# Kernel tuning notes

Hardware: AMD Instinct MI355X
Metric: run time of the kernel (lower is better)

Reference implementation:

```python
import jax, jax.numpy as jnp
import numpy as np

E = 1024   # emb_dim
H = 1024   # hidden_size
L = 2      # num_layers
V = 50257  # vocab_size
S = 2048   # encoder input length
T = 2048   # decoder target length


def setup_inputs() -> dict:
    key = jax.random.key(0)
    ks = jax.random.split(key, 16)
    s = 0.02  # init scale
    f32 = jnp.float32
    return {
        "inputs": jax.random.randint(ks[0], (1, S), 0, V),
        "outputs": jax.random.randint(ks[1], (1, T), 0, V),
        "sos": 1,
        "enc_emb": jax.random.normal(ks[2], (V, E), f32) * s,
        "dec_emb": jax.random.normal(ks[3], (V, E), f32) * s,
        # Stacked LSTM weights; layer-0 input dim == E == H so layers stack.
        "enc_Wih": jax.random.normal(ks[4], (L, 4 * H, H), f32) * s,
        "enc_Whh": jax.random.normal(ks[5], (L, 4 * H, H), f32) * s,
        "enc_bih": jax.random.normal(ks[6], (L, 4 * H), f32) * s,
        "enc_bhh": jax.random.normal(ks[7], (L, 4 * H), f32) * s,
        "dec_Wih": jax.random.normal(ks[8], (L, 4 * H, H), f32) * s,
        "dec_Whh": jax.random.normal(ks[9], (L, 4 * H, H), f32) * s,
        "dec_bih": jax.random.normal(ks[10], (L, 4 * H), f32) * s,
        "dec_bhh": jax.random.normal(ks[11], (L, 4 * H), f32) * s,
        "lin_W": jax.random.normal(ks[12], (V, H), f32) * s,
        "lin_b": jax.random.normal(ks[13], (V,), f32) * s,
    }


def _run_stack(xs, Wih, Whh, bih, bhh, h0, c0):
    # xs: [S, E]; Wih/Whh: [L, 4H, H]; h0/c0: [L, H]
    # PyTorch LSTM gate order: i, f, g, o.
    h_fin, c_fin = [], []
    for l in range(Wih.shape[0]):
        Wi, Wh, bi, bh = Wih[l], Whh[l], bih[l], bhh[l]

        def step(carry, x, Wi=Wi, Wh=Wh, bi=bi, bh=bh):
            h, c = carry
            g = Wi @ x + bi + Wh @ h + bh           # [4H]
            i, f, gg, o = jnp.split(g, 4)
            c = jax.nn.sigmoid(f) * c + jax.nn.sigmoid(i) * jnp.tanh(gg)
            h = jax.nn.sigmoid(o) * jnp.tanh(c)
            return (h, c), h

        (h, c), xs = jax.lax.scan(step, (h0[l], c0[l]), xs)
        h_fin.append(h)
        c_fin.append(c)
    return xs, jnp.stack(h_fin), jnp.stack(c_fin)


def reference(inputs, outputs, sos, enc_emb, dec_emb,
              enc_Wih, enc_Whh, enc_bih, enc_bhh,
              dec_Wih, dec_Whh, dec_bih, dec_bhh,
              lin_W, lin_b):
    # Encoder over the source sequence (batch == 1, squeezed away).
    x = enc_emb[inputs[0]]                       # [S, E]
    z = jnp.zeros((L, H), dtype=x.dtype)
    _, hN, cN = _run_stack(x, enc_Wih, enc_Whh, enc_bih, enc_bhh, z, z)
    # Full teacher forcing: decoder inputs are [sos, outputs[:, :-1]].
    dec_tokens = jnp.concatenate(
        [jnp.array([sos], dtype=outputs.dtype), outputs[0, :-1]])
    y = dec_emb[dec_tokens]                      # [T, E]
    dec_out, _, _ = _run_stack(y, dec_Wih, dec_Whh, dec_bih, dec_bhh, hN, cN)
    logits = dec_out @ lin_W.T + lin_b           # [T, V]
    return logits
```

## Files before the change

### kernel.cpp

```cpp
#include <hip/hip_runtime.h>
#include <hip/hip_bf16.h>
#include <math.h>

#define S_LEN 2048
#define T_LEN 2048
#define HID   1024
#define GATES 4096
#define VOCAB 50257
#define NWG2  192
#define RECT  512

typedef unsigned long long ull;

__device__ __forceinline__ float sigmoidf_(float x) { return 1.0f / (1.0f + expf(-x)); }

__global__ void zero_f32(float* __restrict__ p, int n) {
  int i = blockIdx.x * blockDim.x + threadIdx.x;
  if (i < n) p[i] = 0.0f;
}

__global__ void zero_f4(float4* __restrict__ p, size_t n4) {
  size_t i = (size_t)blockIdx.x * blockDim.x + threadIdx.x;
  size_t stride = (size_t)gridDim.x * blockDim.x;
  for (; i < n4; i += stride) p[i] = make_float4(0.f, 0.f, 0.f, 0.f);
}

__global__ void build_dec_tokens(const int* __restrict__ outputs, const int* __restrict__ sos,
                                 int* __restrict__ toks, int T) {
  int t = blockIdx.x * blockDim.x + threadIdx.x;
  if (t < T) toks[t] = (t == 0) ? sos[0] : outputs[t - 1];
}

__global__ void gather_rows(const float* __restrict__ emb, const int* __restrict__ toks,
                            float* __restrict__ out) {
  int row = blockIdx.x;
  int tok = toks[row];
  const float4* src = (const float4*)(emb + (size_t)tok * HID);
  float4* dst = (float4*)(out + (size_t)row * HID);
  dst[threadIdx.x] = src[threadIdx.x];
}

__global__ __launch_bounds__(256) void gemm_xwt(
    const float* __restrict__ X, const float* __restrict__ W,
    const float* __restrict__ b1, const float* __restrict__ b2,
    float* __restrict__ C, int M, int N, int K)
{
  __shared__ float Xs[16][68];
  __shared__ float Ws[16][68];
  const int tid = threadIdx.x;
  const int tx = tid & 15;
  const int ty = tid >> 4;
  const int m0 = blockIdx.y * 64;
  const int n0 = blockIdx.x * 64;
  const int lr = tid >> 2;
  const int lc = (tid & 3) * 4;
  float acc[4][4] = {{0.f}};

  for (int k0 = 0; k0 < K; k0 += 16) {
    float4 xv = *(const float4*)(X + (size_t)(m0 + lr) * K + k0 + lc);
    float4 wv = make_float4(0.f, 0.f, 0.f, 0.f);
    int wr = n0 + lr;
    if (wr < N) wv = *(const float4*)(W + (size_t)wr * K + k0 + lc);
    __syncthreads();
    Xs[lc + 0][lr] = xv.x; Xs[lc + 1][lr] = xv.y; Xs[lc + 2][lr] = xv.z; Xs[lc + 3][lr] = xv.w;
    Ws[lc + 0][lr] = wv.x; Ws[lc + 1][lr] = wv.y; Ws[lc + 2][lr] = wv.z; Ws[lc + 3][lr] = wv.w;
    __syncthreads();
#pragma unroll
    for (int kk = 0; kk < 16; ++kk) {
      float4 a = *(const float4*)&Xs[kk][ty * 4];
      float4 b = *(const float4*)&Ws[kk][tx * 4];
      float av[4] = {a.x, a.y, a.z, a.w};
      float bv[4] = {b.x, b.y, b.z, b.w};
#pragma unroll
      for (int i = 0; i < 4; ++i)
#pragma unroll
        for (int j = 0; j < 4; ++j)
          acc[i][j] = fmaf(av[i], bv[j], acc[i][j]);
    }
  }
#pragma unroll
  for (int i = 0; i < 4; ++i) {
    int m = m0 + ty * 4 + i;
#pragma unroll
    for (int j = 0; j < 4; ++j) {
      int n = n0 + tx * 4 + j;
      if (n < N) {
        float bias = 0.f;
        if (b1) bias += b1[n];
        if (b2) bias += b2[n];
        C[(size_t)m * N + n] = acc[i][j] + bias;
      }
    }
  }
}

__global__ __launch_bounds__(RECT, 2) void lstm2(
    const float* __restrict__ A,   const float* __restrict__ Wh0,
    const float* __restrict__ Wi1, const float* __restrict__ Wh1,
    const float* __restrict__ bi1, const float* __restrict__ bh1,
    const float* __restrict__ h00, const float* __restrict__ c00,
    const float* __restrict__ h01, const float* __restrict__ c01,
    ull* __restrict__ s0, ull* __restrict__ s1,
    float* __restrict__ hf0, float* __restrict__ cf0,
    float* __restrict__ hf1, float* __restrict__ cf1,
    float* __restrict__ dec_out, int T)
{
  const int tid = threadIdx.x;
  const int wg = blockIdx.x;

  __shared__ float lds_x[HID];
  __shared__ float lds_h[HID];
  __shared__ float lds_g[64];
  __shared__ float lds_c[16];

  if (wg < 64) {
    const int lane8 = tid & 7;
    const int rloc = tid >> 3;
    const int jloc = rloc & 15;
    const int gate = rloc >> 4;
    const int grow = gate * HID + wg * 16 + jloc;

    float4 Wr[32];
    {
      const float4* wrow = (const float4*)(Wh0 + (size_t)grow * HID);
#pragma unroll
      for (int i = 0; i < 32; ++i) Wr[i] = wrow[lane8 + i * 8];
    }

    if (tid < 16) lds_c[tid] = c00[wg * 16 + tid];
    if (tid < 256) ((float4*)lds_h)[tid] = ((const float4*)h00)[tid];
    __syncthreads();

    float areg = (lane8 == 0) ? A[grow] : 0.f;

    for (int t = 0; t < T; ++t) {
      if (t > 0) {
        const ull* hb = s0 + (size_t)(t - 1) * HID;
        ull v0 = __hip_atomic_load(&hb[2 * tid],     __ATOMIC_RELAXED, __HIP_MEMORY_SCOPE_AGENT);
        ull v1 = __hip_atomic_load(&hb[2 * tid + 1], __ATOMIC_RELAXED, __HIP_MEMORY_SCOPE_AGENT);
        while ((unsigned)(v0 >> 32) < (unsigned)t)
          v0 = __hip_atomic_load(&hb[2 * tid],     __ATOMIC_RELAXED, __HIP_MEMORY_SCOPE_AGENT);
        while ((unsigned)(v1 >> 32) < (unsigned)t)
          v1 = __hip_atomic_load(&hb[2 * tid + 1], __ATOMIC_RELAXED, __HIP_MEMORY_SCOPE_AGENT);
        lds_h[2 * tid]     = __uint_as_float((unsigned)v0);
        lds_h[2 * tid + 1] = __uint_as_float((unsigned)v1);
        __syncthreads();
      }

      const float aval = areg;
      if (lane8 == 0 && t + 1 < T) areg = A[(size_t)(t + 1) * GATES + grow];

      float p0 = 0.f, p1 = 0.f, p2 = 0.f, p3 = 0.f;
#pragma unroll
      for (int i = 0; i < 32; ++i) {
        const float4 hv = *(const float4*)&lds_h[(lane8 << 2) + (i << 5)];
        p0 = fmaf(Wr[i].x, hv.x, p0);
        p1 = fmaf(Wr[i].y, hv.y, p1);
        p2 = fmaf(Wr[i].z, hv.z, p2);
        p3 = fmaf(Wr[i].w, hv.w, p3);
      }
      float sum = (p0 + p1) + (p2 + p3);
      sum += __shfl_xor(sum, 1);
      sum += __shfl_xor(sum, 2);
      sum += __shfl_xor(sum, 4);
      if (lane8 == 0) lds_g[rloc] = sum + aval;
      __syncthreads();

      if (tid < 16) {
        const float gi = lds_g[tid];
        const float gf = lds_g[16 + tid];
        const float gg = lds_g[32 + tid];
        const float go = lds_g[48 + tid];
        const float c = sigmoidf_(gf) * lds_c[tid] + sigmoidf_(gi) * tanhf(gg);
        const float h = sigmoidf_(go) * tanhf(c);
        lds_c[tid] = c;
        const int col = wg * 16 + tid;
        const ull pk = ((ull)(unsigned)(t + 1) << 32) | (ull)__float_as_uint(h);
        __hip_atomic_store(&s0[(size_t)t * HID + col], pk,
                           __ATOMIC_RELAXED, __HIP_MEMORY_SCOPE_AGENT);
        if (t == T - 1) {
          if (hf0) hf0[col] = h;
          if (cf0) cf0[col] = c;
        }
      }
    }
  } else {
    const int wg1 = wg - 64;
    const int lane16 = tid & 15;
    const int rloc = tid >> 4;
    const int jloc = rloc & 7;
    const int gate = rloc >> 3;
    const int grow = gate * HID + wg1 * 8 + jloc;

    float4 Wir[16], Whr[16];
    {
      const float4* wi = (const float4*)(Wi1 + (size_t)grow * HID);
      const float4* wh = (const float4*)(Wh1 + (size_t)grow * HID);
#pragma unroll
      for (int i = 0; i < 16; ++i) {
        Wir[i] = wi[lane16 + i * 16];
        Whr[i] = wh[lane16 + i * 16];
      }
    }
    const float breg = bi1[grow] + bh1[grow];

    if (tid < 8) lds_c[tid] = c01[wg1 * 8 + tid];
    if (tid < 256) ((float4*)lds_h)[tid] = ((const float4*)h01)[tid];
    __syncthreads();

    for (int t = 0; t < T; ++t) {
      if (t > 0) {
        const ull* hb = s1 + (size_t)(t - 1) * HID;
        ull v0 = __hip_atomic_load(&hb[2 * tid],     __ATOMIC_RELAXED, __HIP_MEMORY_SCOPE_AGENT);
        ull v1 = __hip_atomic_load(&hb[2 * tid + 1], __ATOMIC_RELAXED, __HIP_MEMORY_SCOPE_AGENT);
        while ((unsigned)(v0 >> 32) < (unsigned)t)
          v0 = __hip_atomic_load(&hb[2 * tid],     __ATOMIC_RELAXED, __HIP_MEMORY_SCOPE_AGENT);
        while ((unsigned)(v1 >> 32) < (unsigned)t)
          v1 = __hip_atomic_load(&hb[2 * tid + 1], __ATOMIC_RELAXED, __HIP_MEMORY_SCOPE_AGENT);
        lds_h[2 * tid]     = __uint_as_float((unsigned)v0);
        lds_h[2 * tid + 1] = __uint_as_float((unsigned)v1);
      }
      {
        const ull* xb = s0 + (size_t)t * HID;
        ull v0 = __hip_atomic_load(&xb[2 * tid],     __ATOMIC_RELAXED, __HIP_MEMORY_SCOPE_AGENT);
        ull v1 = __hip_atomic_load(&xb[2 * tid + 1], __ATOMIC_RELAXED, __HIP_MEMORY_SCOPE_AGENT);
        while ((unsigned)(v0 >> 32) < (unsigned)(t + 1))
          v0 = __hip_atomic_load(&xb[2 * tid],     __ATOMIC_RELAXED, __HIP_MEMORY_SCOPE_AGENT);
        while ((unsigned)(v1 >> 32) < (unsigned)(t + 1))
          v1 = __hip_atomic_load(&xb[2 * tid + 1], __ATOMIC_RELAXED, __HIP_MEMORY_SCOPE_AGENT);
        lds_x[2 * tid]     = __uint_as_float((unsigned)v0);
        lds_x[2 * tid + 1] = __uint_as_float((unsigned)v1);
      }
      __syncthreads();

      float p0 = 0.f, p1 = 0.f, p2 = 0.f, p3 = 0.f;
#pragma unroll
      for (int i = 0; i < 16; ++i) {
        const float4 hv = *(const float4*)&lds_h[(lane16 << 2) + (i << 6)];
        p0 = fmaf(Whr[i].x, hv.x, p0);
        p1 = fmaf(Whr[i].y, hv.y, p1);
        p2 = fmaf(Whr[i].z, hv.z, p2);
        p3 = fmaf(Whr[i].w, hv.w, p3);
      }
#pragma unroll
      for (int i = 0; i < 16; ++i) {
        const float4 xv = *(const float4*)&lds_x[(lane16 << 2) + (i << 6)];
        p0 = fmaf(Wir[i].x, xv.x, p0);
        p1 = fmaf(Wir[i].y, xv.y, p1);
        p2 = fmaf(Wir[i].z, xv.z, p2);
        p3 = fmaf(Wir[i].w, xv.w, p3);
      }
      float sum = (p0 + p1) + (p2 + p3);
      sum += __shfl_xor(sum, 1);
      sum += __shfl_xor(sum, 2);
      sum += __shfl_xor(sum, 4);
      sum += __shfl_xor(sum, 8);
      if (lane16 == 0) lds_g[rloc] = sum + breg;
      __syncthreads();

      if (tid < 8) {
        const float gi = lds_g[tid];
        const float gf = lds_g[8 + tid];
        const float gg = lds_g[16 + tid];
        const float go = lds_g[24 + tid];
        const float c = sigmoidf_(gf) * lds_c[tid] + sigmoidf_(gi) * tanhf(gg);
        const float h = sigmoidf_(go) * tanhf(c);
        lds_c[tid] = c;
        const int col = wg1 * 8 + tid;
        const ull pk = ((ull)(unsigned)(t + 1) << 32) | (ull)__float_as_uint(h);
        __hip_atomic_store(&s1[(size_t)t * HID + col], pk,
                           __ATOMIC_RELAXED, __HIP_MEMORY_SCOPE_AGENT);
        if (dec_out) dec_out[(size_t)t * HID + col] = h;
        if (t == T - 1) {
          if (hf1) hf1[col] = h;
          if (cf1) cf1[col] = c;
        }
      }
    }
  }
}

extern "C" void kernel_launch(void* const* d_in, const int* in_sizes, int n_in,
                              void* d_out, int out_size, void* d_ws, size_t ws_size,
                              hipStream_t stream) {
  const int*   inputs  = (const int*)d_in[0];
  const int*   outputs = (const int*)d_in[1];
  const int*   sos     = (const int*)d_in[2];
  const float* enc_emb = (const float*)d_in[3];
  const float* dec_emb = (const float*)d_in[4];
  const float* enc_Wih = (const float*)d_in[5];
  const float* enc_Whh = (const float*)d_in[6];
  const float* enc_bih = (const float*)d_in[7];
  const float* enc_bhh = (const float*)d_in[8];
  const float* dec_Wih = (const float*)d_in[9];
  const float* dec_Whh = (const float*)d_in[10];
  const float* dec_bih = (const float*)d_in[11];
  const float* dec_bhh = (const float*)d_in[12];
  const float* lin_W   = (const float*)d_in[13];
  const float* lin_b   = (const float*)d_in[14];

  float* out = (float*)d_out;
  float* A_enc = out;
  float* A_dec = out + 8388608;
  ull*   s0e   = (ull*)(out + 16777216);
  ull*   s1e   = s0e + 2097152;
  ull*   s0d   = s1e + 2097152;
  ull*   s1d   = s0d + 2097152;

  char* ws = (char*)d_ws;
  float* zerosv = (float*)(ws + 0);
  float* hf0    = (float*)(ws + 4096);
  float* cf0    = (float*)(ws + 8192);
  float* hf1    = (float*)(ws + 12288);
  float* cf1    = (float*)(ws + 16384);
  int*   dtoks  = (int*)(ws + 20480);
  float* B1 = (float*)(ws + ((size_t)1  << 20));
  float* B3 = (float*)(ws + ((size_t)10 << 20));
  float* B2 = (float*)(ws + ((size_t)19 << 20));

  const size_t WOFF = (size_t)GATES * HID;
  const dim3 gemm_blk(256);
  const dim3 gemmA_grid(GATES / 64, S_LEN / 64);
  const dim3 gemmV_grid((VOCAB + 63) / 64, T_LEN / 64);

  zero_f4<<<2048, 256, 0, stream>>>((float4*)(out + 16777216), 4194304);
  zero_f32<<<4, 256, 0, stream>>>(zerosv, 1024);
  build_dec_tokens<<<8, 256, 0, stream>>>(outputs, sos, dtoks, T_LEN);

  gather_rows<<<S_LEN, 256, 0, stream>>>(enc_emb, inputs, B1);
  gemm_xwt<<<gemmA_grid, gemm_blk, 0, stream>>>(B1, enc_Wih, enc_bih, enc_bhh, A_enc, S_LEN, GATES, HID);
  gather_rows<<<T_LEN, 256, 0, stream>>>(dec_emb, dtoks, B3);
  gemm_xwt<<<gemmA_grid, gemm_blk, 0, stream>>>(B3, dec_Wih, dec_bih, dec_bhh, A_dec, T_LEN, GATES, HID);

  lstm2<<<NWG2, RECT, 0, stream>>>(
      A_enc, enc_Whh, enc_Wih + WOFF, enc_Whh + WOFF, enc_bih + GATES, enc_bhh + GATES,
      zerosv, zerosv, zerosv, zerosv, s0e, s1e, hf0, cf0, hf1, cf1, nullptr, S_LEN);

  lstm2<<<NWG2, RECT, 0, stream>>>(
      A_dec, dec_Whh, dec_Wih + WOFF, dec_Whh + WOFF, dec_bih + GATES, dec_bhh + GATES,
      hf0, cf0, hf1, cf1, s0d, s1d, nullptr, nullptr, nullptr, nullptr, B2, T_LEN);

  gemm_xwt<<<gemmV_grid, gemm_blk, 0, stream>>>(B2, lin_W, lin_b, nullptr, out, T_LEN, VOCAB, HID);
}
```

Before: 13.97 ms.

## Replace per-element tagged h exchange with per-workgroup flags and vector loads

The cross-workgroup handoff of hidden states changes from 64-bit value+step words, each polled by a spin loop, to plain float arrays plus one ready flag per workgroup per step. Consumers spin on a single flag and then fetch four floats with one cache-bypassing dwordx4 load, so each step moves less data and issues fewer atomic polls. Producers wait for their stores to complete before raising the flag, which adds ordering cost on the store side. Gate activations also switch to fast __expf-based sigmoid and tanh, which can lose some accuracy.

```diff
diff --git a/kernel.cpp b/kernel.cpp
--- a/kernel.cpp
+++ b/kernel.cpp
@@ -10,19 +10,21 @@
 #define NWG2  192
 #define RECT  512
 
-typedef unsigned long long ull;
-
-__device__ __forceinline__ float sigmoidf_(float x) { return 1.0f / (1.0f + expf(-x)); }
-
-__global__ void zero_f32(float* __restrict__ p, int n) {
+typedef unsigned int u32;
+
+__device__ __forceinline__ float fsig_(float x)  { return 1.0f / (1.0f + __expf(-x)); }
+__device__ __forceinline__ float ftanh_(float x) { float e = __expf(2.0f * x); return 1.0f - 2.0f / (e + 1.0f); }
+
+__device__ __forceinline__ float4 load_coherent4(const float* p) {
+  float4 v;
+  asm volatile("global_load_dwordx4 %0, %1, off sc0 sc1\n\ts_waitcnt vmcnt(0)"
+               : "=v"(v) : "v"(p) : "memory");
+  return v;
+}
+
+__global__ void zero_u32(u32* __restrict__ p, int n) {
   int i = blockIdx.x * blockDim.x + threadIdx.x;
-  if (i < n) p[i] = 0.0f;
-}
-
-__global__ void zero_f4(float4* __restrict__ p, size_t n4) {
-  size_t i = (size_t)blockIdx.x * blockDim.x + threadIdx.x;
-  size_t stride = (size_t)gridDim.x * blockDim.x;
-  for (; i < n4; i += stride) p[i] = make_float4(0.f, 0.f, 0.f, 0.f);
+  if (i < n) p[i] = 0u;
 }
 
 __global__ void build_dec_tokens(const int* __restrict__ outputs, const int* __restrict__ sos,
@@ -100,7 +102,8 @@
     const float* __restrict__ bi1, const float* __restrict__ bh1,
     const float* __restrict__ h00, const float* __restrict__ c00,
     const float* __restrict__ h01, const float* __restrict__ c01,
-    ull* __restrict__ s0, ull* __restrict__ s1,
+    float* __restrict__ s0, float* __restrict__ s1,
+    u32* __restrict__ t0, u32* __restrict__ t1,
     float* __restrict__ hf0, float* __restrict__ cf0,
     float* __restrict__ hf1, float* __restrict__ cf1,
     float* __restrict__ dec_out, int T)
@@ -135,15 +138,13 @@
 
     for (int t = 0; t < T; ++t) {
       if (t > 0) {
-        const ull* hb = s0 + (size_t)(t - 1) * HID;
-        ull v0 = __hip_atomic_load(&hb[2 * tid],     __ATOMIC_RELAXED, __HIP_MEMORY_SCOPE_AGENT);
-        ull v1 = __hip_atomic_load(&hb[2 * tid + 1], __ATOMIC_RELAXED, __HIP_MEMORY_SCOPE_AGENT);
-        while ((unsigned)(v0 >> 32) < (unsigned)t)
-          v0 = __hip_atomic_load(&hb[2 * tid],     __ATOMIC_RELAXED, __HIP_MEMORY_SCOPE_AGENT);
-        while ((unsigned)(v1 >> 32) < (unsigned)t)
-          v1 = __hip_atomic_load(&hb[2 * tid + 1], __ATOMIC_RELAXED, __HIP_MEMORY_SCOPE_AGENT);
-        lds_h[2 * tid]     = __uint_as_float((unsigned)v0);
-        lds_h[2 * tid + 1] = __uint_as_float((unsigned)v1);
+        if (tid < 256) {
+          const int c4 = tid << 2;
+          const u32* tg = t0 + (size_t)(t - 1) * 64 + (c4 >> 4);
+          while (__hip_atomic_load(tg, __ATOMIC_RELAXED, __HIP_MEMORY_SCOPE_AGENT) < (u32)t) {}
+          const float4 v = load_coherent4(s0 + (size_t)(t - 1) * HID + c4);
+          *(float4*)&lds_h[c4] = v;
+        }
         __syncthreads();
       }
 
@@ -171,17 +172,20 @@
         const float gf = lds_g[16 + tid];
         const float gg = lds_g[32 + tid];
         const float go = lds_g[48 + tid];
-        const float c = sigmoidf_(gf) * lds_c[tid] + sigmoidf_(gi) * tanhf(gg);
-        const float h = sigmoidf_(go) * tanhf(c);
+        const float c = fsig_(gf) * lds_c[tid] + fsig_(gi) * ftanh_(gg);
+        const float h = fsig_(go) * ftanh_(c);
         lds_c[tid] = c;
         const int col = wg * 16 + tid;
-        const ull pk = ((ull)(unsigned)(t + 1) << 32) | (ull)__float_as_uint(h);
-        __hip_atomic_store(&s0[(size_t)t * HID + col], pk,
+        __hip_atomic_store((u32*)&s0[(size_t)t * HID + col], __float_as_uint(h),
                            __ATOMIC_RELAXED, __HIP_MEMORY_SCOPE_AGENT);
         if (t == T - 1) {
           if (hf0) hf0[col] = h;
           if (cf0) cf0[col] = c;
         }
+        asm volatile("s_waitcnt vmcnt(0)" ::: "memory");
+        if (tid == 0)
+          __hip_atomic_store(&t0[(size_t)t * 64 + wg], (u32)(t + 1),
+                             __ATOMIC_RELAXED, __HIP_MEMORY_SCOPE_AGENT);
       }
     }
   } else {
@@ -209,27 +213,19 @@
     __syncthreads();
 
     for (int t = 0; t < T; ++t) {
-      if (t > 0) {
-        const ull* hb = s1 + (size_t)(t - 1) * HID;
-        ull v0 = __hip_atomic_load(&hb[2 * tid],     __ATOMIC_RELAXED, __HIP_MEMORY_SCOPE_AGENT);
-        ull v1 = __hip_atomic_load(&hb[2 * tid + 1], __ATOMIC_RELAXED, __HIP_MEMORY_SCOPE_AGENT);
-        while ((unsigned)(v0 >> 32) < (unsigned)t)
-          v0 = __hip_atomic_load(&hb[2 * tid],     __ATOMIC_RELAXED, __HIP_MEMORY_SCOPE_AGENT);
-        while ((unsigned)(v1 >> 32) < (unsigned)t)
-          v1 = __hip_atomic_load(&hb[2 * tid + 1], __ATOMIC_RELAXED, __HIP_MEMORY_SCOPE_AGENT);
-        lds_h[2 * tid]     = __uint_as_float((unsigned)v0);
-        lds_h[2 * tid + 1] = __uint_as_float((unsigned)v1);
-      }
-      {
-        const ull* xb = s0 + (size_t)t * HID;
-        ull v0 = __hip_atomic_load(&xb[2 * tid],     __ATOMIC_RELAXED, __HIP_MEMORY_SCOPE_AGENT);
-        ull v1 = __hip_atomic_load(&xb[2 * tid + 1], __ATOMIC_RELAXED, __HIP_MEMORY_SCOPE_AGENT);
-        while ((unsigned)(v0 >> 32) < (unsigned)(t + 1))
-          v0 = __hip_atomic_load(&xb[2 * tid],     __ATOMIC_RELAXED, __HIP_MEMORY_SCOPE_AGENT);
-        while ((unsigned)(v1 >> 32) < (unsigned)(t + 1))
-          v1 = __hip_atomic_load(&xb[2 * tid + 1], __ATOMIC_RELAXED, __HIP_MEMORY_SCOPE_AGENT);
-        lds_x[2 * tid]     = __uint_as_float((unsigned)v0);
-        lds_x[2 * tid + 1] = __uint_as_float((unsigned)v1);
+      if (tid < 256) {
+        const int c4 = tid << 2;
+        const u32* tg = t0 + (size_t)t * 64 + (c4 >> 4);
+        while (__hip_atomic_load(tg, __ATOMIC_RELAXED, __HIP_MEMORY_SCOPE_AGENT) < (u32)(t + 1)) {}
+        const float4 v = load_coherent4(s0 + (size_t)t * HID + c4);
+        *(float4*)&lds_x[c4] = v;
+      } else if (t > 0) {
+        const int u = tid - 256;
+        const int c4 = u << 2;
+        const u32* tg = t1 + (size_t)(t - 1) * 128 + (u >> 1);
+        while (__hip_atomic_load(tg, __ATOMIC_RELAXED, __HIP_MEMORY_SCOPE_AGENT) < (u32)t) {}
+        const float4 v = load_coherent4(s1 + (size_t)(t - 1) * HID + c4);
+        *(float4*)&lds_h[c4] = v;
       }
       __syncthreads();
 
@@ -263,18 +259,21 @@
         const float gf = lds_g[8 + tid];
         const float gg = lds_g[16 + tid];
         const float go = lds_g[24 + tid];
-        const float c = sigmoidf_(gf) * lds_c[tid] + sigmoidf_(gi) * tanhf(gg);
-        const float h = sigmoidf_(go) * tanhf(c);
+        const float c = fsig_(gf) * lds_c[tid] + fsig_(gi) * ftanh_(gg);
+        const float h = fsig_(go) * ftanh_(c);
         lds_c[tid] = c;
         const int col = wg1 * 8 + tid;
-        const ull pk = ((ull)(unsigned)(t + 1) << 32) | (ull)__float_as_uint(h);
-        __hip_atomic_store(&s1[(size_t)t * HID + col], pk,
+        __hip_atomic_store((u32*)&s1[(size_t)t * HID + col], __float_as_uint(h),
                            __ATOMIC_RELAXED, __HIP_MEMORY_SCOPE_AGENT);
         if (dec_out) dec_out[(size_t)t * HID + col] = h;
         if (t == T - 1) {
           if (hf1) hf1[col] = h;
           if (cf1) cf1[col] = c;
         }
+        asm volatile("s_waitcnt vmcnt(0)" ::: "memory");
+        if (tid == 0)
+          __hip_atomic_store(&t1[(size_t)t * 128 + wg1], (u32)(t + 1),
+                             __ATOMIC_RELAXED, __HIP_MEMORY_SCOPE_AGENT);
       }
     }
   }
@@ -302,10 +301,16 @@
   float* out = (float*)d_out;
   float* A_enc = out;
   float* A_dec = out + 8388608;
-  ull*   s0e   = (ull*)(out + 16777216);
-  ull*   s1e   = s0e + 2097152;
-  ull*   s0d   = s1e + 2097152;
-  ull*   s1d   = s0d + 2097152;
+  float* s0e   = out + 16777216;
+  float* s1e   = s0e + 2097152;
+  float* s0d   = s1e + 2097152;
+  float* s1d   = s0d + 2097152;
+  u32*   tagsB = (u32*)(out + 25165824);
+  u32*   t0e = tagsB;
+  u32*   t1e = t0e + 2048 * 64;
+  u32*   t0d = t1e + 2048 * 128;
+  u32*   t1d = t0d + 2048 * 64;
+  const int NTAGS = 2048 * 384;
 
   char* ws = (char*)d_ws;
   float* zerosv = (float*)(ws + 0);
@@ -323,8 +328,8 @@
   const dim3 gemmA_grid(GATES / 64, S_LEN / 64);
   const dim3 gemmV_grid((VOCAB + 63) / 64, T_LEN / 64);
 
-  zero_f4<<<2048, 256, 0, stream>>>((float4*)(out + 16777216), 4194304);
-  zero_f32<<<4, 256, 0, stream>>>(zerosv, 1024);
+  zero_u32<<<(NTAGS + 255) / 256, 256, 0, stream>>>(tagsB, NTAGS);
+  zero_u32<<<4, 256, 0, stream>>>((u32*)zerosv, 1024);
   build_dec_tokens<<<8, 256, 0, stream>>>(outputs, sos, dtoks, T_LEN);
 
   gather_rows<<<S_LEN, 256, 0, stream>>>(enc_emb, inputs, B1);
@@ -334,11 +339,11 @@
 
   lstm2<<<NWG2, RECT, 0, stream>>>(
       A_enc, enc_Whh, enc_Wih + WOFF, enc_Whh + WOFF, enc_bih + GATES, enc_bhh + GATES,
-      zerosv, zerosv, zerosv, zerosv, s0e, s1e, hf0, cf0, hf1, cf1, nullptr, S_LEN);
+      zerosv, zerosv, zerosv, zerosv, s0e, s1e, t0e, t1e, hf0, cf0, hf1, cf1, nullptr, S_LEN);
 
   lstm2<<<NWG2, RECT, 0, stream>>>(
       A_dec, dec_Whh, dec_Wih + WOFF, dec_Whh + WOFF, dec_bih + GATES, dec_bhh + GATES,
-      hf0, cf0, hf1, cf1, s0d, s1d, nullptr, nullptr, nullptr, nullptr, B2, T_LEN);
+      hf0, cf0, hf1, cf1, s0d, s1d, t0d, t1d, nullptr, nullptr, nullptr, nullptr, B2, T_LEN);
 
   gemm_xwt<<<gemmV_grid, gemm_blk, 0, stream>>>(B2, lin_W, lin_b, nullptr, out, T_LEN, VOCAB, HID);
 }
```

Result: slower. 26.13 ms (+87.1%).
